# Kernel optimization log

Hardware: AMD Instinct MI355X
Metric: run time of the kernel (lower is better)

Reference implementation:

```python
import jax, jax.numpy as jnp
import numpy as np


def setup_inputs() -> dict:
    key = jax.random.key(0)
    k1, k2, k3 = jax.random.split(key, 3)
    b_n, f_num, N = 2, 4, 50
    n = b_n * f_num
    C_in, C = 256, 64
    h, w = 200, 336
    return {
        "x": jax.random.normal(k1, (n, C, h * w), jnp.float32),
        "idx_feat": jax.random.normal(k2, (n, C_in, N, 1), jnp.float32),
        "weight": jax.random.normal(k3, (C, C_in), jnp.float32) * 0.01,
        "bias": jnp.zeros((C,), jnp.float32),
        "thing_gt_idx": jnp.ones((b_n, N, f_num), jnp.int32),
        "h": h,
        "w": w,
    }


def _con_loss(mw, b_n, N, f_num, C):
    # mw: (b_n*f_num, C, N, 1) kernel embeddings after embed_extractor
    K = N * f_num
    # reshape/permute mirrors torch: (b_n, N, f_num, C) flattened row-major ->
    # rows ordered (instance, frame), matching the boolean-mask gather order
    # under a dense (all-ones) thing_gt_idx mask.
    m = mw.reshape(b_n, f_num, C, N).transpose(0, 3, 1, 2).reshape(b_n, K, C)
    # F.normalize(dim=1)
    m = m / jnp.maximum(jnp.linalg.norm(m, axis=-1, keepdims=True), 1e-12)
    sim = jnp.einsum('bkc,blc->bkl', m, m)  # (b_n, K, K)
    labels = np.repeat(np.arange(N), f_num)  # instance id per row (static)
    f_own = np.tile(np.arange(f_num), N)     # frame id per row (static)
    # static negative gather indices: all columns of other instances, padded by
    # repeating the last negative (torch's while-loop torch.cat) to length K-1
    neg_cols = []
    for i in range(N):
        cols = np.nonzero(labels != i)[0]
        neg_cols.append(np.concatenate([cols, np.full(f_num - 1, cols[-1])]))
    neg_idx = np.stack(neg_cols)[labels]     # (K, K-1)
    # random positive among the f_num-1 same-instance / other-frame entries
    r = jax.random.randint(jax.random.key(42), (b_n, K), 0, f_num - 1)
    pos_off = jnp.where(r >= f_own[None, :], r + 1, r)
    pos_col = labels[None, :] * f_num + pos_off  # (b_n, K)
    positives = sim[jnp.arange(b_n)[:, None], jnp.arange(K)[None, :], pos_col]
    negatives = sim[:, np.arange(K)[:, None], neg_idx]  # (b_n, K, K-1)
    logits = jnp.concatenate([positives[..., None], negatives], axis=-1) / 0.07
    # CrossEntropyLoss with target 0, mean over K rows, summed over batches
    lse = jax.scipy.special.logsumexp(logits, axis=-1)
    return jnp.sum(jnp.mean(lse - logits[..., 0], axis=-1))


def reference(x, idx_feat, weight, bias, thing_gt_idx, h, w):
    b_n, N, f_num = thing_gt_idx.shape
    n = b_n * f_num
    C = weight.shape[0]
    # embed_extractor: 1x1 conv == channel matmul
    mw = jnp.einsum('bcnk,dc->bdnk', idx_feat, weight) + bias[None, :, None, None]
    loss = _con_loss(mw, b_n, N, f_num, C)
    # shuffle_times == 1 branch: kernels @ encoded features
    kernels = mw.reshape(n, C, N).transpose(0, 2, 1)  # (n, N, C)
    inst_pred = jnp.matmul(kernels, x).reshape(n, N, h, w)
    return inst_pred, loss
```

## Files before the change

### kernel.cpp

```cpp
#include <hip/hip_runtime.h>
#include <stdint.h>
#include <float.h>
#include <math.h>

#define HW_TOT 67200
#define NBF 8
#define CO 64
#define CI 256
#define NN 50
#define KK 200
#define BN 2

__device__ __forceinline__ uint32_t rotl32(uint32_t v, int n) {
  return (v << n) | (v >> (32 - n));
}

__device__ void tf2x32(uint32_t k0, uint32_t k1, uint32_t x0, uint32_t x1,
                       uint32_t& o0, uint32_t& o1) {
  const uint32_t ks2 = k0 ^ k1 ^ 0x1BD11BDAu;
  x0 += k0; x1 += k1;
  x0 += x1; x1 = rotl32(x1, 13); x1 ^= x0;
  x0 += x1; x1 = rotl32(x1, 15); x1 ^= x0;
  x0 += x1; x1 = rotl32(x1, 26); x1 ^= x0;
  x0 += x1; x1 = rotl32(x1, 6);  x1 ^= x0;
  x0 += k1; x1 += ks2 + 1u;
  x0 += x1; x1 = rotl32(x1, 17); x1 ^= x0;
  x0 += x1; x1 = rotl32(x1, 29); x1 ^= x0;
  x0 += x1; x1 = rotl32(x1, 16); x1 ^= x0;
  x0 += x1; x1 = rotl32(x1, 24); x1 ^= x0;
  x0 += ks2; x1 += k0 + 2u;
  x0 += x1; x1 = rotl32(x1, 13); x1 ^= x0;
  x0 += x1; x1 = rotl32(x1, 15); x1 ^= x0;
  x0 += x1; x1 = rotl32(x1, 26); x1 ^= x0;
  x0 += x1; x1 = rotl32(x1, 6);  x1 ^= x0;
  x0 += k0; x1 += k1 + 3u;
  x0 += x1; x1 = rotl32(x1, 17); x1 ^= x0;
  x0 += x1; x1 = rotl32(x1, 29); x1 ^= x0;
  x0 += x1; x1 = rotl32(x1, 16); x1 ^= x0;
  x0 += x1; x1 = rotl32(x1, 24); x1 ^= x0;
  x0 += k1; x1 += ks2 + 4u;
  x0 += x1; x1 = rotl32(x1, 13); x1 ^= x0;
  x0 += x1; x1 = rotl32(x1, 15); x1 ^= x0;
  x0 += x1; x1 = rotl32(x1, 26); x1 ^= x0;
  x0 += x1; x1 = rotl32(x1, 6);  x1 ^= x0;
  o0 = x0 + ks2;
  o1 = x1 + k0 + 5u;
}

__device__ int jax_r(int b, int k) {
  uint32_t k1a, k1b, k2a, k2b, h0, h1, l0, l1;
  tf2x32(0u, 42u, 0u, 0u, k1a, k1b);
  tf2x32(0u, 42u, 0u, 1u, k2a, k2b);
  const uint32_t idx = (uint32_t)(b * KK + k);
  tf2x32(k1a, k1b, 0u, idx, h0, h1);
  tf2x32(k2a, k2b, 0u, idx, l0, l1);
  const uint32_t hb = h0 ^ h1, lb = l0 ^ l1;
  return (int)(((hb % 3u) + (lb % 3u)) % 3u);
}

__global__ __launch_bounds__(256) void k_mw(const float* __restrict__ idx_feat,
                                            const float* __restrict__ weight,
                                            const float* __restrict__ bias,
                                            float* __restrict__ mw) {
  const int tid = blockIdx.x * 256 + threadIdx.x;
  if (tid >= NBF * CO * NN) return;
  const int n = tid % NN;
  const int rest = tid / NN;
  const int d = rest % CO;
  const int b = rest / CO;
  float acc = bias[d];
  const float* feat = idx_feat + (size_t)(b * CI) * NN + n;
  const float* wrow = weight + d * CI;
  #pragma unroll 8
  for (int ci = 0; ci < CI; ++ci)
    acc = fmaf(feat[ci * NN], wrow[ci], acc);
  mw[tid] = acc;
}

__device__ __forceinline__ float waveMax(float v) {
  #pragma unroll
  for (int o = 32; o > 0; o >>= 1) v = fmaxf(v, __shfl_down(v, o));
  return v;
}
__device__ __forceinline__ float waveSum(float v) {
  #pragma unroll
  for (int o = 32; o > 0; o >>= 1) v += __shfl_down(v, o);
  return v;
}

__global__ __launch_bounds__(256) void k_loss(const float* __restrict__ mw,
                                              float* __restrict__ partial) {
  __shared__ __align__(16) float m_lds[KK][68];
  __shared__ float red[8];
  __shared__ float pos_sh;
  __shared__ int rvals[32];

  const int b = blockIdx.x >> 3;
  const int chunk = blockIdx.x & 7;
  const int t = threadIdx.x;
  const int wid = t >> 6, lane = t & 63;
  const int kbase = chunk * 25;

  if (t < 25) rvals[t] = jax_r(b, kbase + t);

  float row[CO];
  if (t < KK) {
    const int f = t & 3, ni = t >> 2;
    const float* src = mw + (size_t)((b * 4 + f) * CO) * NN + ni;
    float ssq = 0.f;
    #pragma unroll
    for (int c = 0; c < CO; ++c) { const float v = src[c * NN]; row[c] = v; ssq += v * v; }
    const float inv = 1.0f / fmaxf(sqrtf(ssq), 1e-12f);
    #pragma unroll
    for (int c = 0; c < CO; ++c) { row[c] *= inv; m_lds[t][c] = row[c]; }
  }
  __syncthreads();

  float part = 0.f;
  for (int kk = 0; kk < 25; ++kk) {
    const int k = kbase + kk;
    const int g = k >> 2, fo = k & 3;
    const int r = rvals[kk];
    const int pos_off = (r >= fo) ? r + 1 : r;
    const int pos_col = (g << 2) + pos_off;
    const int last_neg = (g == NN - 1) ? (KK - 5) : (KK - 1);

    float dot = 0.f;
    if (t < KK) {
      const float4* mk = reinterpret_cast<const float4*>(&m_lds[k][0]);
      #pragma unroll
      for (int c4 = 0; c4 < 16; ++c4) {
        const float4 a = mk[c4];
        dot = fmaf(a.x, row[4 * c4 + 0], dot);
        dot = fmaf(a.y, row[4 * c4 + 1], dot);
        dot = fmaf(a.z, row[4 * c4 + 2], dot);
        dot = fmaf(a.w, row[4 * c4 + 3], dot);
      }
    }
    const float logit = dot * (1.0f / 0.07f);

    float wgt = 0.f;
    if (t < KK) {
      if (t == pos_col) wgt = 1.f;
      else if ((t >> 2) != g) wgt = (t == last_neg) ? 4.f : 1.f;
    }
    const bool valid = wgt > 0.f;

    const float wmax = waveMax(valid ? logit : -FLT_MAX);
    if (lane == 0) red[wid] = wmax;
    if (t == pos_col) pos_sh = logit;
    __syncthreads();
    const float mx = fmaxf(fmaxf(red[0], red[1]), fmaxf(red[2], red[3]));
    const float pos = pos_sh;
    const float ws = waveSum(valid ? wgt * expf(logit - mx) : 0.f);
    if (lane == 0) red[4 + wid] = ws;
    __syncthreads();
    if (t == 0) {
      const float s = red[4] + red[5] + red[6] + red[7];
      part += (mx + logf(s)) - pos;
    }
    __syncthreads();
  }
  if (t == 0) partial[blockIdx.x] = part;
}

__global__ __launch_bounds__(256) void k_pred(const float* __restrict__ x,
                                              const float* __restrict__ mw,
                                              const float* __restrict__ partial,
                                              float* __restrict__ out) {
  const int b = blockIdx.y;
  const int p = blockIdx.x * 256 + threadIdx.x;

  if (blockIdx.x == 0 && b == 0 && threadIdx.x == 0) {
    float s = 0.f;
    #pragma unroll
    for (int i = 0; i < 16; ++i) s += partial[i];
    out[(size_t)NBF * NN * HW_TOT] = s * (1.0f / KK);
  }
  if (p >= HW_TOT) return;

  float acc[NN];
  #pragma unroll
  for (int i = 0; i < NN; ++i) acc[i] = 0.f;

  const float* xb = x + (size_t)b * CO * HW_TOT + p;
  const float* mwb = mw + b * CO * NN;
  for (int c = 0; c < CO; ++c) {
    const float xv = xb[(size_t)c * HW_TOT];
    const float* kr = mwb + c * NN;
    #pragma unroll
    for (int ni = 0; ni < NN; ++ni)
      acc[ni] = fmaf(kr[ni], xv, acc[ni]);
  }

  float* ob = out + (size_t)b * NN * HW_TOT + p;
  #pragma unroll
  for (int ni = 0; ni < NN; ++ni)
    ob[(size_t)ni * HW_TOT] = acc[ni];
}

extern "C" void kernel_launch(void* const* d_in, const int* in_sizes, int n_in,
                              void* d_out, int out_size, void* d_ws, size_t ws_size,
                              hipStream_t stream) {
  const float* x        = (const float*)d_in[0];
  const float* idx_feat = (const float*)d_in[1];
  const float* weight   = (const float*)d_in[2];
  const float* bias     = (const float*)d_in[3];
  float* out = (float*)d_out;

  float* mw = (float*)d_ws;
  float* partial = mw + NBF * CO * NN;

  hipLaunchKernelGGL(k_mw, dim3((NBF * CO * NN + 255) / 256), dim3(256), 0, stream,
                     idx_feat, weight, bias, mw);
  hipLaunchKernelGGL(k_loss, dim3(16), dim3(256), 0, stream, mw, partial);
  hipLaunchKernelGGL(k_pred, dim3((HW_TOT + 255) / 256, NBF), dim3(256), 0, stream,
                     x, mw, partial, out);
}
```

Measured before the change: 96.53 us.

## Rewrite prediction matmul with bf16 MFMA tiles staged through swizzled LDS

New measurement: 92.49 us. 1.04x faster.

```diff
diff --git a/kernel.cpp b/kernel.cpp
--- a/kernel.cpp
+++ b/kernel.cpp
@@ -164,39 +164,99 @@
   if (t == 0) partial[blockIdx.x] = part;
 }
 
-__global__ __launch_bounds__(256) void k_pred(const float* __restrict__ x,
-                                              const float* __restrict__ mw,
-                                              const float* __restrict__ partial,
-                                              float* __restrict__ out) {
+typedef __attribute__((ext_vector_type(8))) short bf16x8;
+typedef __attribute__((ext_vector_type(4))) float f32x4;
+
+__device__ __forceinline__ uint32_t bf16rne(float f) {
+  uint32_t u = __builtin_bit_cast(uint32_t, f);
+  return (u + 0x7FFFu + ((u >> 16) & 1u)) >> 16;
+}
+
+__global__ __launch_bounds__(256, 4) void k_pred(const float* __restrict__ x,
+                                                 const float* __restrict__ mw,
+                                                 const float* __restrict__ partial,
+                                                 float* __restrict__ out) {
+  __shared__ __align__(16) char lds[64 * 128];
+
   const int b = blockIdx.y;
-  const int p = blockIdx.x * 256 + threadIdx.x;
-
-  if (blockIdx.x == 0 && b == 0 && threadIdx.x == 0) {
+  const int p0 = blockIdx.x * 64;
+  const int u = threadIdx.x;
+  const int l = u & 63;
+  const int w = u >> 6;
+  const int ln = l & 15, lg = l >> 4;
+
+  const float* xb  = x  + (size_t)b * CO * HW_TOT;
+  const float* mwb = mw + (size_t)b * CO * NN;
+
+  const int sc0 = 4 * (u >> 4);
+  const int sp0 = 4 * (u & 15);
+  const float4 v0 = *reinterpret_cast<const float4*>(xb + (size_t)(sc0 + 0) * HW_TOT + p0 + sp0);
+  const float4 v1 = *reinterpret_cast<const float4*>(xb + (size_t)(sc0 + 1) * HW_TOT + p0 + sp0);
+  const float4 v2 = *reinterpret_cast<const float4*>(xb + (size_t)(sc0 + 2) * HW_TOT + p0 + sp0);
+  const float4 v3 = *reinterpret_cast<const float4*>(xb + (size_t)(sc0 + 3) * HW_TOT + p0 + sp0);
+
+  bf16x8 afr[2];
+  #pragma unroll
+  for (int ks = 0; ks < 2; ++ks) {
+    #pragma unroll
+    for (int j = 0; j < 8; ++j) {
+      const int c = ks * 32 + lg * 8 + j;
+      const int n = min(16 * w + ln, NN - 1);
+      afr[ks][j] = (short)bf16rne(mwb[c * NN + n]);
+    }
+  }
+
+  {
+    const float c0s[4] = {v0.x, v1.x, v2.x, v3.x};
+    const float c1s[4] = {v0.y, v1.y, v2.y, v3.y};
+    const float c2s[4] = {v0.z, v1.z, v2.z, v3.z};
+    const float c3s[4] = {v0.w, v1.w, v2.w, v3.w};
+    const float* cols[4] = {c0s, c1s, c2s, c3s};
+    #pragma unroll
+    for (int s = 0; s < 4; ++s) {
+      const float* cv = cols[s];
+      const uint32_t lo = bf16rne(cv[0]) | (bf16rne(cv[1]) << 16);
+      const uint32_t hi = bf16rne(cv[2]) | (bf16rne(cv[3]) << 16);
+      const int row = sp0 + s;
+      const int wb = (row * 128 + sc0 * 2) ^ ((row & 7) << 4);
+      *reinterpret_cast<uint2*>(lds + wb) = make_uint2(lo, hi);
+    }
+  }
+  __syncthreads();
+
+  f32x4 acc[4];
+  #pragma unroll
+  for (int q = 0; q < 4; ++q) acc[q] = (f32x4){0.f, 0.f, 0.f, 0.f};
+
+  #pragma unroll
+  for (int ks = 0; ks < 2; ++ks) {
+    #pragma unroll
+    for (int q = 0; q < 4; ++q) {
+      const int row = q * 16 + ln;
+      const int rb = (row * 128 + ks * 64 + lg * 16) ^ ((ln & 7) << 4);
+      const uint4 raw = *reinterpret_cast<const uint4*>(lds + rb);
+      const bf16x8 bfr = __builtin_bit_cast(bf16x8, raw);
+      acc[q] = __builtin_amdgcn_mfma_f32_16x16x32_bf16(afr[ks], bfr, acc[q], 0, 0, 0);
+    }
+  }
+
+  float* ob = out + (size_t)b * NN * HW_TOT + p0;
+  #pragma unroll
+  for (int q = 0; q < 4; ++q) {
+    #pragma unroll
+    for (int i = 0; i < 4; ++i) {
+      const int n = 16 * w + 4 * lg + i;
+      if (n < NN)
+        __builtin_nontemporal_store(acc[q][i], ob + (size_t)n * HW_TOT + q * 16 + ln);
+    }
+  }
+
+  if (blockIdx.x == 0 && b == 0 && u == 0) {
     float s = 0.f;
     #pragma unroll
     for (int i = 0; i < 16; ++i) s += partial[i];
     out[(size_t)NBF * NN * HW_TOT] = s * (1.0f / KK);
   }
-  if (p >= HW_TOT) return;
-
-  float acc[NN];
-  #pragma unroll
-  for (int i = 0; i < NN; ++i) acc[i] = 0.f;
-
-  const float* xb = x + (size_t)b * CO * HW_TOT + p;
-  const float* mwb = mw + b * CO * NN;
-  for (int c = 0; c < CO; ++c) {
-    const float xv = xb[(size_t)c * HW_TOT];
-    const float* kr = mwb + c * NN;
-    #pragma unroll
-    for (int ni = 0; ni < NN; ++ni)
-      acc[ni] = fmaf(kr[ni], xv, acc[ni]);
-  }
-
-  float* ob = out + (size_t)b * NN * HW_TOT + p;
-  #pragma unroll
-  for (int ni = 0; ni < NN; ++ni)
-    ob[(size_t)ni * HW_TOT] = acc[ni];
 }
 
 extern "C" void kernel_launch(void* const* d_in, const int* in_sizes, int n_in,
@@ -214,6 +274,6 @@
   hipLaunchKernelGGL(k_mw, dim3((NBF * CO * NN + 255) / 256), dim3(256), 0, stream,
                      idx_feat, weight, bias, mw);
   hipLaunchKernelGGL(k_loss, dim3(16), dim3(256), 0, stream, mw, partial);
-  hipLaunchKernelGGL(k_pred, dim3((HW_TOT + 255) / 256, NBF), dim3(256), 0, stream,
+  hipLaunchKernelGGL(k_pred, dim3(HW_TOT / 64, NBF), dim3(256), 0, stream,
                      x, mw, partial, out);
 }
```

## Use bf16 MFMA for prediction matmul with LDS transpose and nontemporal stores

Applied to the files above, without the earlier changes.

After: 85.31 us. -11.6%, faster.

```diff
diff --git a/kernel.cpp b/kernel.cpp
--- a/kernel.cpp
+++ b/kernel.cpp
@@ -164,39 +164,107 @@
   if (t == 0) partial[blockIdx.x] = part;
 }
 
-__global__ __launch_bounds__(256) void k_pred(const float* __restrict__ x,
-                                              const float* __restrict__ mw,
-                                              const float* __restrict__ partial,
-                                              float* __restrict__ out) {
+typedef __attribute__((ext_vector_type(8))) short bf16x8;
+typedef __attribute__((ext_vector_type(4))) float f32x4;
+
+__device__ __forceinline__ uint32_t bf16rne(float f) {
+  uint32_t u = __builtin_bit_cast(uint32_t, f);
+  return (u + 0x7FFFu + ((u >> 16) & 1u)) >> 16;
+}
+
+__global__ __launch_bounds__(64, 3) void k_pred(const float* __restrict__ x,
+                                                const float* __restrict__ mw,
+                                                const float* __restrict__ partial,
+                                                float* __restrict__ out) {
+  __shared__ __align__(16) char wlds[64 * 136];
+
   const int b = blockIdx.y;
-  const int p = blockIdx.x * 256 + threadIdx.x;
-
-  if (blockIdx.x == 0 && b == 0 && threadIdx.x == 0) {
+  const int p0 = blockIdx.x * 64;
+  const int l = threadIdx.x;
+  const int ln = l & 15, lg = l >> 4;
+
+  const float* xb  = x  + (size_t)b * CO * HW_TOT + p0 + l;
+  const float* mwb = mw + (size_t)b * CO * NN;
+
+  bf16x8 afr[4][2];
+  #pragma unroll
+  for (int ns = 0; ns < 4; ++ns) {
+    const int n = min(ns * 16 + ln, NN - 1);
+    #pragma unroll
+    for (int ks = 0; ks < 2; ++ks)
+      #pragma unroll
+      for (int j = 0; j < 8; ++j)
+        afr[ns][ks][j] = (short)bf16rne(mwb[(ks * 32 + lg * 8 + j) * NN + n]);
+  }
+
+  float xr[64];
+  #pragma unroll
+  for (int c = 0; c < 64; ++c)
+    xr[c] = xb[(size_t)c * HW_TOT];
+
+  #pragma unroll
+  for (int c = 0; c < 64; c += 2) {
+    const uint32_t pk = bf16rne(xr[c]) | (bf16rne(xr[c + 1]) << 16);
+    *reinterpret_cast<uint32_t*>(wlds + l * 136 + c * 2) = pk;
+  }
+
+  f32x4 acc[4][4];
+  #pragma unroll
+  for (int ns = 0; ns < 4; ++ns)
+    #pragma unroll
+    for (int q = 0; q < 4; ++q) acc[ns][q] = (f32x4){0.f, 0.f, 0.f, 0.f};
+
+  #pragma unroll
+  for (int ks = 0; ks < 2; ++ks) {
+    #pragma unroll
+    for (int q = 0; q < 4; ++q) {
+      const bf16x8 bfr = *reinterpret_cast<const bf16x8*>(
+          wlds + (q * 16 + ln) * 136 + (ks * 32 + lg * 8) * 2);
+      #pragma unroll
+      for (int ns = 0; ns < 4; ++ns)
+        acc[ns][q] = __builtin_amdgcn_mfma_f32_16x16x32_bf16(afr[ns][ks], bfr,
+                                                             acc[ns][q], 0, 0, 0);
+    }
+  }
+
+  asm volatile("s_waitcnt lgkmcnt(0)" ::: "memory");
+  __builtin_amdgcn_sched_barrier(0);
+
+  float* ot = reinterpret_cast<float*>(wlds);
+  float* ob = out + (size_t)b * NN * HW_TOT + p0 + l;
+
+  #pragma unroll
+  for (int half = 0; half < 2; ++half) {
+    #pragma unroll
+    for (int ns = 0; ns < 2; ++ns)
+      #pragma unroll
+      for (int q = 0; q < 4; ++q)
+        #pragma unroll
+        for (int i = 0; i < 4; ++i)
+          ot[(ns * 16 + 4 * lg + i) * 68 + q * 16 + ln] = acc[half * 2 + ns][q][i];
+
+    asm volatile("s_waitcnt lgkmcnt(0)" ::: "memory");
+    __builtin_amdgcn_sched_barrier(0);
+
+    #pragma unroll
+    for (int r = 0; r < 32; ++r) {
+      const int n = half * 32 + r;
+      if (n < NN)
+        __builtin_nontemporal_store(ot[r * 68 + l], ob + (size_t)n * HW_TOT);
+    }
+
+    if (half == 0) {
+      asm volatile("s_waitcnt lgkmcnt(0)" ::: "memory");
+      __builtin_amdgcn_sched_barrier(0);
+    }
+  }
+
+  if (blockIdx.x == 0 && b == 0 && l == 0) {
     float s = 0.f;
     #pragma unroll
     for (int i = 0; i < 16; ++i) s += partial[i];
     out[(size_t)NBF * NN * HW_TOT] = s * (1.0f / KK);
   }
-  if (p >= HW_TOT) return;
-
-  float acc[NN];
-  #pragma unroll
-  for (int i = 0; i < NN; ++i) acc[i] = 0.f;
-
-  const float* xb = x + (size_t)b * CO * HW_TOT + p;
-  const float* mwb = mw + b * CO * NN;
-  for (int c = 0; c < CO; ++c) {
-    const float xv = xb[(size_t)c * HW_TOT];
-    const float* kr = mwb + c * NN;
-    #pragma unroll
-    for (int ni = 0; ni < NN; ++ni)
-      acc[ni] = fmaf(kr[ni], xv, acc[ni]);
-  }
-
-  float* ob = out + (size_t)b * NN * HW_TOT + p;
-  #pragma unroll
-  for (int ni = 0; ni < NN; ++ni)
-    ob[(size_t)ni * HW_TOT] = acc[ni];
 }
 
 extern "C" void kernel_launch(void* const* d_in, const int* in_sizes, int n_in,
@@ -214,6 +282,6 @@
   hipLaunchKernelGGL(k_mw, dim3((NBF * CO * NN + 255) / 256), dim3(256), 0, stream,
                      idx_feat, weight, bias, mw);
   hipLaunchKernelGGL(k_loss, dim3(16), dim3(256), 0, stream, mw, partial);
-  hipLaunchKernelGGL(k_pred, dim3((HW_TOT + 255) / 256, NBF), dim3(256), 0, stream,
+  hipLaunchKernelGGL(k_pred, dim3(HW_TOT / 64, NBF), dim3(64), 0, stream,
                      x, mw, partial, out);
 }
```
